# Optimization experiments

Hardware: AMD Instinct MI355X
Metric: run time of the kernel (lower is better)

Reference implementation:

```python
import jax, jax.numpy as jnp
import numpy as np

C0 = 16          # embed channels (c0) == mamba d_model
OUT_DIM = 32
D_INNER = 32     # expand * c0
D_STATE = 16
D_CONV = 4
DT_RANK = 1      # max(1, d_model // 16)
EPS = 1e-5


def setup_inputs():
    key = jax.random.key(0)
    ks = jax.random.split(key, 32)

    def n(i, shape, s):
        return (jax.random.normal(ks[i], shape) * s).astype(jnp.float32)

    inp = {
        "x": jax.random.normal(ks[0], (1, 4, 64, 64, 64), jnp.float32),
        "embed_w": n(1, (4, C0, 1, 7, 7, 7), 0.1),   # 4 per-modality conv7 stems
        "ln_g": jnp.ones((C0,), jnp.float32),
        "ln_b": jnp.zeros((C0,), jnp.float32),
        "in_proj_w": n(2, (2 * D_INNER, C0), 0.25),
        "out_proj_w": n(3, (C0, D_INNER), 0.18),
        "up_w": n(4, (C0, OUT_DIM, 2, 2, 2), 0.2),   # ConvTranspose3d k=2 s=2
    }
    for j, sfx in enumerate(["", "_b"]):             # forward / backward scan params
        b = 5 + 7 * j
        inp["conv_w" + sfx] = n(b, (D_INNER, 1, D_CONV), 0.3)
        inp["conv_b" + sfx] = n(b + 1, (D_INNER,), 0.1)
        inp["xproj_w" + sfx] = n(b + 2, (DT_RANK + 2 * D_STATE, D_INNER), 0.15)
        inp["dtproj_w" + sfx] = n(b + 3, (D_INNER, DT_RANK), 0.5)
        inp["dtproj_b" + sfx] = jnp.full((D_INNER,), -4.6, jnp.float32)  # softplus ~= 0.01
        inp["A_log" + sfx] = jnp.log(jnp.tile(jnp.arange(1, D_STATE + 1, dtype=jnp.float32), (D_INNER, 1)))
        inp["D_skip" + sfx] = jnp.ones((D_INNER,), jnp.float32)
    return inp


def _instnorm(x):
    m = jnp.mean(x, axis=(2, 3, 4), keepdims=True)
    v = jnp.mean(jnp.square(x - m), axis=(2, 3, 4), keepdims=True)
    return (x - m) / jnp.sqrt(v + EPS)


def _embed(x1, w):
    # Conv3d(1, c0, k=7, s=2, p=3, bias=False) -> InstanceNorm3d -> GELU(exact)
    y = jax.lax.conv_general_dilated(x1, w, (2, 2, 2), [(3, 3)] * 3,
                                     dimension_numbers=('NCDHW', 'OIDHW', 'NCDHW'))
    return jax.nn.gelu(_instnorm(y), approximate=False)


def _branch(u, z, cw, cb, xw, dtw, dtb, A_log, D_skip):
    # One Mamba scan branch. u, z: [B, L, Dn]
    Dn = u.shape[-1]
    uc = jax.lax.conv_general_dilated(jnp.swapaxes(u, 1, 2), cw, (1,), [(D_CONV - 1, 0)],
                                      feature_group_count=Dn,
                                      dimension_numbers=('NCH', 'OIH', 'NCH'))
    u = jax.nn.silu(jnp.swapaxes(uc + cb[None, :, None], 1, 2))       # causal dw-conv + SiLU
    xdbl = u @ xw.T                                                   # [B,L,R+2N]
    dt = jax.nn.softplus(xdbl[..., :DT_RANK] @ dtw.T + dtb)           # [B,L,Dn]
    Bm = xdbl[..., DT_RANK:DT_RANK + D_STATE]                         # [B,L,N]
    Cm = xdbl[..., DT_RANK + D_STATE:]                                # [B,L,N]
    A = -jnp.exp(A_log)                                               # [Dn,N]
    a = jnp.exp(dt[..., None] * A)                                    # [B,L,Dn,N]
    b = (dt * u)[..., None] * Bm[:, :, None, :]                       # [B,L,Dn,N]

    def comb(c1, c2):
        a1, b1 = c1
        a2, b2 = c2
        return a1 * a2, a2 * b1 + b2

    _, h = jax.lax.associative_scan(comb, (a, b), axis=1)             # h_t = a_t h_{t-1} + b_t
    y = jnp.einsum('bldn,bln->bld', h, Cm) + u * D_skip
    return y * jax.nn.silu(z)


def _bimamba(t, p):
    xz = t @ p['in_proj_w'].T
    xi, z = jnp.split(xz, 2, axis=-1)
    yf = _branch(xi, z, p['conv_w'], p['conv_b'], p['xproj_w'], p['dtproj_w'],
                 p['dtproj_b'], p['A_log'], p['D_skip'])
    yb = _branch(xi[:, ::-1], z[:, ::-1], p['conv_w_b'], p['conv_b_b'], p['xproj_w_b'],
                 p['dtproj_w_b'], p['dtproj_b_b'], p['A_log_b'], p['D_skip_b'])[:, ::-1]
    return (yf + yb) @ p['out_proj_w'].T


def _mamba_dir(x5, p):
    B, C = x5.shape[:2]
    t = jnp.swapaxes(x5.reshape(B, C, -1), 1, 2)                      # [B, L, C]
    mu = jnp.mean(t, axis=-1, keepdims=True)
    var = jnp.mean(jnp.square(t - mu), axis=-1, keepdims=True)
    t = (t - mu) / jnp.sqrt(var + EPS) * p['ln_g'] + p['ln_b']        # LayerNorm
    t = _bimamba(t, p)
    return jnp.swapaxes(t, 1, 2).reshape(x5.shape)


def _mamba_layer(x5, p):
    # tri-directional scans: (d,w,h), (w,d,h), (h,w,d) + residual
    o1 = _mamba_dir(x5, p)
    o2 = jnp.transpose(_mamba_dir(jnp.transpose(x5, (0, 1, 3, 2, 4)), p), (0, 1, 3, 2, 4))
    o3 = jnp.transpose(_mamba_dir(jnp.transpose(x5, (0, 1, 4, 3, 2)), p), (0, 1, 4, 3, 2))
    return o1 + o2 + o3 + x5


def reference(x, embed_w, ln_g, ln_b, in_proj_w, out_proj_w, up_w,
              conv_w, conv_b, xproj_w, dtproj_w, dtproj_b, A_log, D_skip,
              conv_w_b, conv_b_b, xproj_w_b, dtproj_w_b, dtproj_b_b, A_log_b, D_skip_b):
    p = dict(ln_g=ln_g, ln_b=ln_b, in_proj_w=in_proj_w, out_proj_w=out_proj_w,
             conv_w=conv_w, conv_b=conv_b, xproj_w=xproj_w, dtproj_w=dtproj_w,
             dtproj_b=dtproj_b, A_log=A_log, D_skip=D_skip,
             conv_w_b=conv_w_b, conv_b_b=conv_b_b, xproj_w_b=xproj_w_b,
             dtproj_w_b=dtproj_w_b, dtproj_b_b=dtproj_b_b, A_log_b=A_log_b,
             D_skip_b=D_skip_b)
    us = [_embed(x[:, m:m + 1], embed_w[m]) for m in range(4)]        # 4 modalities
    outs = [_mamba_layer(u, p) for u in us]
    y = outs[0] + outs[1] + outs[2] + outs[3] + us[0] + us[1] + us[2] + us[3]
    B, _, D, H, W = y.shape
    # ConvTranspose3d(c0, out_dim, k=2, s=2): each output 2x2x2 block from one input voxel
    y = jnp.einsum('bcdhw,coijk->bodihjwk', y, up_w).reshape(B, OUT_DIM, 2 * D, 2 * H, 2 * W)
    return y
```

## Files before the change

kernel.cpp:

```cpp
#include <hip/hip_runtime.h>
#include <math.h>

#define L 32768
#define CH 64
#define NC 512

#if __has_builtin(__builtin_amdgcn_exp2f)
#define EXP2(x) __builtin_amdgcn_exp2f(x)
#else
#define EXP2(x) exp2f(x)
#endif

__device__ __forceinline__ int sigma_map(int l, int perm) {
    int b2 = l >> 10, b1 = (l >> 5) & 31, b0 = l & 31;
    if (perm == 0) return (b2 << 10) | (b1 << 5) | b0;
    if (perm == 1) return (b1 << 10) | (b2 << 5) | b0;
    return (b0 << 10) | (b1 << 5) | b2;
}

__device__ __forceinline__ float silu_f(float v) {
    return v / (1.f + __expf(-v));
}
__device__ __forceinline__ float softplus_f(float x) {
    return fmaxf(x, 0.f) + log1pf(__expf(-fabsf(x)));
}

__device__ __forceinline__ float oct_sum(float x) {
    int v = __builtin_amdgcn_update_dpp(0, __float_as_int(x), 0xB1, 0xf, 0xf, true);
    x += __int_as_float(v);
    v = __builtin_amdgcn_update_dpp(0, __float_as_int(x), 0x4E, 0xf, 0xf, true);
    x += __int_as_float(v);
    v = __builtin_amdgcn_update_dpp(0, __float_as_int(x), 0x124, 0xf, 0xf, true);
    x += __int_as_float(v);
    return x;
}

__global__ __launch_bounds__(256) void k_embed(const float* __restrict__ x,
                                               const float* __restrict__ w,
                                               float* __restrict__ us) {
    __shared__ float tile[10143];
    int bx = blockIdx.x, m = blockIdx.y;
    int c = bx >> 7, sb = bx & 127;
    int zc = sb >> 2, yc0 = (sb & 3) << 3;
    const float* xin = x + m * 262144;
    int iz0 = 2 * zc - 3, iy0 = 2 * yc0 - 3;
    for (int i = threadIdx.x; i < 10143; i += 256) {
        int tz = i / 1449, r = i - tz * 1449;
        int ty = r / 69, tx = r - ty * 69;
        int gz = iz0 + tz, gy = iy0 + ty, gx = tx - 3;
        float v = 0.f;
        if ((unsigned)gz < 64u && (unsigned)gy < 64u && (unsigned)gx < 64u)
            v = xin[(gz * 64 + gy) * 64 + gx];
        tile[i] = v;
    }
    __syncthreads();
    const float* wc = w + (m * 16 + c) * 343;
    int tyl = threadIdx.x >> 5, xc = threadIdx.x & 31;
    float acc = 0.f;
    for (int kz = 0; kz < 7; ++kz)
        for (int ky = 0; ky < 7; ++ky) {
            const float* row = &tile[(kz * 21 + 2 * tyl + ky) * 69 + 2 * xc];
            const float* wr = &wc[kz * 49 + ky * 7];
            #pragma unroll
            for (int kx = 0; kx < 7; ++kx) acc += row[kx] * wr[kx];
        }
    us[(m * 16 + c) * 32768 + sb * 256 + threadIdx.x] = acc;
}

__global__ void k_instnorm_gelu(float* __restrict__ us) {
    int ch = blockIdx.x;
    float* p = us + ch * 32768;
    float s = 0.f, s2 = 0.f;
    for (int i = threadIdx.x; i < 32768; i += 256) { float v = p[i]; s += v; s2 += v * v; }
    __shared__ float rs[256], rs2[256];
    rs[threadIdx.x] = s; rs2[threadIdx.x] = s2;
    __syncthreads();
    for (int o = 128; o > 0; o >>= 1) {
        if (threadIdx.x < o) { rs[threadIdx.x] += rs[threadIdx.x + o]; rs2[threadIdx.x] += rs2[threadIdx.x + o]; }
        __syncthreads();
    }
    float mu = rs[0] * (1.f / 32768.f);
    float var = rs2[0] * (1.f / 32768.f) - mu * mu;
    float rinv = rsqrtf(var + 1e-5f);
    for (int i = threadIdx.x; i < 32768; i += 256) {
        float v = (p[i] - mu) * rinv;
        p[i] = 0.5f * v * (1.f + erff(v * 0.70710678118654752f));
    }
}

__global__ void k_transpose(const float* __restrict__ us, float* __restrict__ us_t) {
    __shared__ float tl[16][257];
    int m = blockIdx.x >> 7, t0 = (blockIdx.x & 127) << 8;
    for (int i = threadIdx.x; i < 4096; i += 256) {
        int c = i >> 8, j = i & 255;
        tl[c][j] = us[(m * 16 + c) * 32768 + t0 + j];
    }
    __syncthreads();
    for (int i = threadIdx.x; i < 4096; i += 256) {
        int j = i >> 4, c = i & 15;
        us_t[(m * 32768 + t0 + j) * 16 + c] = tl[c][j];
    }
}

__global__ __launch_bounds__(512) void k_chunkA2(
    const float* __restrict__ us_t, const float* __restrict__ ln_g, const float* __restrict__ ln_b,
    const float* __restrict__ Wip, const float* __restrict__ Wout,
    const float* __restrict__ cwA, const float* __restrict__ cbA, const float* __restrict__ xwA,
    const float* __restrict__ dtwA, const float* __restrict__ dtbA, const float* __restrict__ AlA,
    const float* __restrict__ DsA,
    const float* __restrict__ cwB, const float* __restrict__ cbB, const float* __restrict__ xwB,
    const float* __restrict__ dtwB, const float* __restrict__ dtbB, const float* __restrict__ AlB,
    const float* __restrict__ DsB,
    float* __restrict__ hst, float* __restrict__ sumdtSt,
    float* __restrict__ xd0st, _Float16* __restrict__ Csth,
    float* __restrict__ O) {
    __shared__ float sm[13376];
    float* xiT = sm;
    float* zT  = sm + 2304;
    float* syT = sm + 4480;
    float* uSh = sm + 6656;
    float* sBC = sm + 8832;
    float* xd0 = sm + 11136;
    float* G   = sm + 11200;

    int c = blockIdx.x, dir = blockIdx.y;
    int m = dir / 3, perm = dir - m * 3;
    int p0 = c * CH;
    int tid = threadIdx.x;

    for (int i = tid; i < 1024; i += 512) G[i] = Wip[i];
    if (tid < 16) G[1024 + tid] = ln_g[tid];
    else if (tid < 32) G[1024 + tid] = ln_b[tid - 16];
    __syncthreads();

    if (tid < 70) {
        int p = p0 - 3 + tid;
        if ((unsigned)p < (unsigned)L) {
            int sp = sigma_map(p, perm);
            const float4* rw = (const float4*)(us_t + (m * 32768 + sp) * 16);
            float t[16];
            ((float4*)t)[0] = rw[0]; ((float4*)t)[1] = rw[1];
            ((float4*)t)[2] = rw[2]; ((float4*)t)[3] = rw[3];
            float mu = 0.f;
            #pragma unroll
            for (int ci = 0; ci < 16; ++ci) mu += t[ci];
            mu *= (1.f / 16.f);
            float var = 0.f;
            #pragma unroll
            for (int ci = 0; ci < 16; ++ci) { float d = t[ci] - mu; var += d * d; }
            var *= (1.f / 16.f);
            float rinv = rsqrtf(var + 1e-5f);
            #pragma unroll
            for (int ci = 0; ci < 16; ++ci)
                uSh[ci * 72 + tid] = (t[ci] - mu) * rinv * G[1024 + ci] + G[1040 + ci];
        } else {
            #pragma unroll
            for (int ci = 0; ci < 16; ++ci) uSh[ci * 72 + tid] = 0.f;
        }
    }
    __syncthreads();

    for (int it = tid; it < 1152; it += 512) {
        int dd = it / 18, q = it - dd * 18;
        float ax = 0.f, ay = 0.f, az = 0.f, aw = 0.f;
        #pragma unroll
        for (int ci = 0; ci < 16; ++ci) {
            float4 tq = *(const float4*)&uSh[ci * 72 + 4 * q];
            float wv = G[dd * 16 + ci];
            ax += tq.x * wv; ay += tq.y * wv; az += tq.z * wv; aw += tq.w * wv;
        }
        int d = dd & 31;
        if (dd < 32) {
            float4 o4 = {ax, ay, az, aw};
            *(float4*)&xiT[d * 72 + 4 * q] = o4;
        } else if (q < 17) {
            float4 o4 = {silu_f(ax), silu_f(ay), silu_f(az), silu_f(aw)};
            *(float4*)&zT[d * 68 + 4 * q] = o4;
        }
    }
    __syncthreads();

    for (int b = 0; b < 2; ++b) {
        const float* cw  = b ? cwB  : cwA;
        const float* cb  = b ? cbB  : cbA;
        const float* xw  = b ? xwB  : xwA;
        const float* dtw = b ? dtwB : dtwA;
        const float* dtb = b ? dtbB : dtbA;
        const float* Al  = b ? AlB  : AlA;
        const float* Ds  = b ? DsB  : DsA;
        int chunk = b ? (NC - 1 - c) : c;
        size_t dirbIdx = (size_t)(dir * 2 + b) * NC + chunk;

        for (int i = tid; i < 1056; i += 512) G[i] = xw[i];
        if (tid < 128) G[1056 + tid] = cw[tid];
        else if (tid < 160) G[1056 + tid] = cb[tid - 128];
        __syncthreads();

        {
            int d = tid >> 4, q = tid & 15, s0 = 4 * q;
            float xr[7];
            if (b == 0) {
                #pragma unroll
                for (int j = 0; j < 7; ++j) xr[j] = xiT[d * 72 + s0 + j];
            } else {
                #pragma unroll
                for (int j = 0; j < 7; ++j) xr[j] = xiT[d * 72 + 63 - s0 + j];
            }
            float w0 = G[1056 + d * 4], w1 = G[1057 + d * 4], w2 = G[1058 + d * 4], w3 = G[1059 + d * 4];
            float bias = G[1184 + d];
            #pragma unroll
            for (int i = 0; i < 4; ++i) {
                float a;
                if (b == 0) a = bias + xr[i] * w0 + xr[i + 1] * w1 + xr[i + 2] * w2 + xr[i + 3] * w3;
                else        a = bias + xr[6 - i] * w0 + xr[5 - i] * w1 + xr[4 - i] * w2 + xr[3 - i] * w3;
                uSh[d * 68 + s0 + i] = silu_f(a);
            }
        }
        __syncthreads();

        for (int it = tid; it < 528; it += 512) {
            int j = it >> 4, q = it & 15, s0 = 4 * q;
            float ax = 0.f, ay = 0.f, az = 0.f, aw = 0.f;
            #pragma unroll
            for (int ci = 0; ci < 32; ++ci) {
                float4 uq = *(const float4*)&uSh[ci * 68 + s0];
                float wv = G[j * 32 + ci];
                ax += uq.x * wv; ay += uq.y * wv; az += uq.z * wv; aw += uq.w * wv;
            }
            if (j == 0) {
                float4 o4 = {ax, ay, az, aw};
                *(float4*)&xd0[s0] = o4;
                *(float4*)&xd0st[dirbIdx * 64 + s0] = o4;
            } else {
                int col;
                if (j < 17) { int bj = j - 1;  col = 4 * (bj >> 1) + (bj & 1); }
                else        { int cj = j - 17; col = 4 * (cj >> 1) + 2 + (cj & 1); }
                sBC[(s0 + 0) * 36 + col] = ax;
                sBC[(s0 + 1) * 36 + col] = ay;
                sBC[(s0 + 2) * 36 + col] = az;
                sBC[(s0 + 3) * 36 + col] = aw;
                if (j >= 17) {
                    int cj = j - 17;
                    Csth[(dirbIdx * 64 + s0 + 0) * 16 + cj] = (_Float16)ax;
                    Csth[(dirbIdx * 64 + s0 + 1) * 16 + cj] = (_Float16)ay;
                    Csth[(dirbIdx * 64 + s0 + 2) * 16 + cj] = (_Float16)az;
                    Csth[(dirbIdx * 64 + s0 + 3) * 16 + cj] = (_Float16)aw;
                }
            }
        }
        __syncthreads();

        for (int i = tid; i < 2048; i += 512) {
            int d2 = i >> 6, s = i & 63;
            G[d2 * 68 + s] = softplus_f(xd0[s] * dtw[d2] + dtb[d2]);
        }
        __syncthreads();

        if (tid < 256) {
            int d = tid >> 3, lane8 = tid & 7, nb = lane8 * 2;
            float kk0 = -1.44269504f * __expf(Al[d * 16 + nb + 0]);
            float kk1 = -1.44269504f * __expf(Al[d * 16 + nb + 1]);
            float Dsv = Ds[d];
            float h0 = 0.f, h1 = 0.f, cum = 0.f;
            const float* dtp = &G[d * 68];
            const float* up  = &uSh[d * 68];
            for (int s0 = 0; s0 < CH; s0 += 4) {
                float4 dt4 = *(const float4*)&dtp[s0];
                float4 u4  = *(const float4*)&up[s0];
                float pr0, pr1, pr2, pr3;
                #define CSTEP(DT, UU, SS, PR) { \
                    float w_ = (DT) * (UU); \
                    float4 bc = *(const float4*)&sBC[(SS) * 36 + 4 * lane8]; \
                    h0 = fmaf(EXP2((DT) * kk0), h0, w_ * bc.x); \
                    h1 = fmaf(EXP2((DT) * kk1), h1, w_ * bc.y); \
                    float p_ = fmaf(h1, bc.w, h0 * bc.z); \
                    cum += (DT); \
                    PR = oct_sum(p_); }
                CSTEP(dt4.x, u4.x, s0 + 0, pr0)
                CSTEP(dt4.y, u4.y, s0 + 1, pr1)
                CSTEP(dt4.z, u4.z, s0 + 2, pr2)
                CSTEP(dt4.w, u4.w, s0 + 3, pr3)
                #undef CSTEP
                if (lane8 == 0) {
                    if (b == 0) {
                        float4 o;
                        o.x = pr0 + u4.x * Dsv;
                        o.y = pr1 + u4.y * Dsv;
                        o.z = pr2 + u4.z * Dsv;
                        o.w = pr3 + u4.w * Dsv;
                        *(float4*)&syT[d * 68 + s0] = o;
                    } else {
                        float4* dst = (float4*)&syT[d * 68 + (60 - s0)];
                        float4 o = *dst;
                        o.x += pr3 + u4.w * Dsv;
                        o.y += pr2 + u4.z * Dsv;
                        o.z += pr1 + u4.y * Dsv;
                        o.w += pr0 + u4.x * Dsv;
                        *dst = o;
                    }
                }
            }
            float2 hv; hv.x = h0; hv.y = h1;
            *(float2*)&hst[dirbIdx * 512 + (size_t)(d * 16 + nb)] = hv;
            if (lane8 == 0) sumdtSt[dirbIdx * 32 + d] = cum;
        }
        __syncthreads();
    }

    for (int it = tid; it < 2048; it += 512) {
        int d = it >> 6, pl = it & 63;
        syT[d * 68 + pl] *= zT[d * 68 + pl + 3];
    }
    __syncthreads();

    if (tid < 512) G[tid] = Wout[tid];
    __syncthreads();
    for (int it = tid; it < 1024; it += 512) {
        int p = it >> 4, cc = it & 15;
        float acc = 0.f;
        #pragma unroll
        for (int d = 0; d < 32; ++d) acc += syT[d * 68 + p] * G[cc * 32 + d];
        O[((size_t)(dir * 32768 + p0 + p)) * 16 + cc] = acc;
    }
}

__global__ __launch_bounds__(512) void k_scanB(float* __restrict__ hst,
                                               const float* __restrict__ sumdtSt,
                                               const float* __restrict__ AlA,
                                               const float* __restrict__ AlB) {
    int db = blockIdx.x;
    const float* Al = (db & 1) ? AlB : AlA;
    int t = threadIdx.x, d = t >> 4;
    float A = -__expf(Al[t]);
    float* base = hst + (size_t)db * NC * 512 + t;
    const float* sb = sumdtSt + (size_t)db * NC * 32 + d;
    float H = 0.f;
    for (int c0 = 0; c0 < NC; c0 += 4) {
        float h0 = base[(c0 + 0) * 512], h1 = base[(c0 + 1) * 512];
        float h2 = base[(c0 + 2) * 512], h3 = base[(c0 + 3) * 512];
        float P0 = __expf(sb[(c0 + 0) * 32] * A);
        float P1 = __expf(sb[(c0 + 1) * 32] * A);
        float P2 = __expf(sb[(c0 + 2) * 32] * A);
        float P3 = __expf(sb[(c0 + 3) * 32] * A);
        base[(c0 + 0) * 512] = H; H = fmaf(P0, H, h0);
        base[(c0 + 1) * 512] = H; H = fmaf(P1, H, h1);
        base[(c0 + 2) * 512] = H; H = fmaf(P2, H, h2);
        base[(c0 + 3) * 512] = H; H = fmaf(P3, H, h3);
    }
}

__global__ __launch_bounds__(512) void k_fix(
    const float* __restrict__ us_t, const float* __restrict__ ln_g, const float* __restrict__ ln_b,
    const float* __restrict__ Wip, const float* __restrict__ Wout,
    const float* __restrict__ dtwA, const float* __restrict__ dtbA, const float* __restrict__ AlA,
    const float* __restrict__ dtwB, const float* __restrict__ dtbB, const float* __restrict__ AlB,
    const float* __restrict__ hst, const float* __restrict__ xd0st,
    const _Float16* __restrict__ Csth, float* __restrict__ O) {
    __shared__ float hinF[512], hinB[512];
    __shared__ float CF[1280], CB[1280];
    __shared__ float tnT[1088];
    __shared__ float sWz[512], sWout[512], sgb[32];
    __shared__ float xdF[64], xdB[64];
    __shared__ float cumB[2048];
    __shared__ float lsum[512];
    __shared__ float syC[2176];

    int c = blockIdx.x, dir = blockIdx.y;
    int m = dir / 3, perm = dir - m * 3;
    int tid = threadIdx.x;

    size_t fI = (size_t)(dir * 2 + 0) * NC + c;
    size_t bI = (size_t)(dir * 2 + 1) * NC + (NC - 1 - c);

    hinF[tid] = hst[fI * 512 + tid];
    hinB[tid] = hst[bI * 512 + tid];
    sWz[tid]  = Wip[512 + tid];
    sWout[tid] = Wout[tid];
    if (tid < 16) sgb[tid] = ln_g[tid];
    else if (tid < 32) sgb[tid] = ln_b[tid - 16];
    if (tid < 64) { xdF[tid] = xd0st[fI * 64 + tid]; xdB[tid] = xd0st[bI * 64 + tid]; }
    {
        const _Float16* cf = Csth + fI * 1024;
        const _Float16* cbp = Csth + bI * 1024;
        int i = tid, s = i >> 4, n = i & 15;
        CF[s * 20 + n] = (float)cf[i]; CB[s * 20 + n] = (float)cbp[i];
        i = tid + 512; s = i >> 4; n = i & 15;
        CF[s * 20 + n] = (float)cf[i]; CB[s * 20 + n] = (float)cbp[i];
    }
    __syncthreads();

    if (tid < 64) {
        int p = c * CH + tid;
        int sp = sigma_map(p, perm);
        const float4* rw = (const float4*)(us_t + (m * 32768 + sp) * 16);
        float t[16];
        ((float4*)t)[0] = rw[0]; ((float4*)t)[1] = rw[1];
        ((float4*)t)[2] = rw[2]; ((float4*)t)[3] = rw[3];
        float mu = 0.f;
        #pragma unroll
        for (int ci = 0; ci < 16; ++ci) mu += t[ci];
        mu *= (1.f / 16.f);
        float var = 0.f;
        #pragma unroll
        for (int ci = 0; ci < 16; ++ci) { float dd = t[ci] - mu; var += dd * dd; }
        var *= (1.f / 16.f);
        float rinv = rsqrtf(var + 1e-5f);
        #pragma unroll
        for (int ci = 0; ci < 16; ++ci)
            tnT[ci * 68 + tid] = (t[ci] - mu) * rinv * sgb[ci] + sgb[16 + ci];
    }
    __syncthreads();

    int d = tid >> 4, sq = tid & 15, s0 = 4 * sq;

    float dwF = dtwA[d], dbF = dtbA[d];
    float dF0 = softplus_f(xdF[s0 + 0] * dwF + dbF);
    float dF1 = softplus_f(xdF[s0 + 1] * dwF + dbF);
    float dF2 = softplus_f(xdF[s0 + 2] * dwF + dbF);
    float dF3 = softplus_f(xdF[s0 + 3] * dwF + dbF);
    lsum[tid] = ((dF0 + dF1) + (dF2 + dF3));
    __syncthreads();
    float baseF = 0.f;
    #pragma unroll
    for (int k = 0; k < 16; ++k) { float v = lsum[d * 16 + k]; baseF += (k < sq) ? v : 0.f; }
    float cF0 = baseF + dF0, cF1 = cF0 + dF1, cF2 = cF1 + dF2, cF3 = cF2 + dF3;
    __syncthreads();

    float dwB = dtwB[d], dbB = dtbB[d];
    float dB0 = softplus_f(xdB[s0 + 0] * dwB + dbB);
    float dB1 = softplus_f(xdB[s0 + 1] * dwB + dbB);
    float dB2 = softplus_f(xdB[s0 + 2] * dwB + dbB);
    float dB3 = softplus_f(xdB[s0 + 3] * dwB + dbB);
    lsum[tid] = ((dB0 + dB1) + (dB2 + dB3));
    __syncthreads();
    float baseB = 0.f;
    #pragma unroll
    for (int k = 0; k < 16; ++k) { float v = lsum[d * 16 + k]; baseB += (k < sq) ? v : 0.f; }
    {
        float c0v = baseB + dB0, c1v = c0v + dB1, c2v = c1v + dB2, c3v = c2v + dB3;
        float4 o4 = {c0v, c1v, c2v, c3v};
        *(float4*)&cumB[d * 64 + s0] = o4;
    }
    __syncthreads();

    {
        float z0 = 0.f, z1 = 0.f, z2 = 0.f, z3 = 0.f;
        #pragma unroll
        for (int ci = 0; ci < 16; ++ci) {
            float4 tq = *(const float4*)&tnT[ci * 68 + s0];
            float wv = sWz[d * 16 + ci];
            z0 += tq.x * wv; z1 += tq.y * wv; z2 += tq.z * wv; z3 += tq.w * wv;
        }
        z0 = silu_f(z0); z1 = silu_f(z1); z2 = silu_f(z2); z3 = silu_f(z3);
        float zv[4] = {z0, z1, z2, z3};
        float cFv[4] = {cF0, cF1, cF2, cF3};

        float e0F = __expf(AlA[d * 16]);
        float e0B = __expf(AlB[d * 16]);
        const float* hFp = &hinF[d * 16];
        const float* hBp = &hinB[d * 16];

        float out4[4];
        #pragma unroll
        for (int i = 0; i < 4; ++i) {
            int p = s0 + i;
            int sb = 63 - p;
            float rF = __expf(-cFv[i] * e0F);
            float rB = __expf(-cumB[d * 64 + sb] * e0B);
            const float* Crf = &CF[p * 20];
            const float* Crb = &CB[sb * 20];
            float accF = 0.f, accB = 0.f;
            #pragma unroll
            for (int n = 15; n >= 0; --n) {
                accF = fmaf(rF, accF, hFp[n] * Crf[n]);
                accB = fmaf(rB, accB, hBp[n] * Crb[n]);
            }
            out4[i] = (rF * accF + rB * accB) * zv[i];
        }
        float4 o4 = {out4[0], out4[1], out4[2], out4[3]};
        *(float4*)&syC[d * 68 + s0] = o4;
    }
    __syncthreads();

    for (int it = tid; it < 1024; it += 512) {
        int p = it >> 4, cc2 = it & 15;
        float acc = 0.f;
        #pragma unroll
        for (int dd = 0; dd < 32; ++dd) acc += syC[dd * 68 + p] * sWout[cc2 * 32 + dd];
        size_t oi = ((size_t)(dir * 32768 + c * CH + p)) * 16 + cc2;
        O[oi] += acc;
    }
}

__global__ void k_accum(const float* __restrict__ us_t, const float* __restrict__ O,
                        float* __restrict__ acc_t) {
    int it = blockIdx.x * 256 + threadIdx.x;
    int sp = it >> 2, q = (it & 3) << 2;
    float ax = 0.f, ay = 0.f, az = 0.f, aw = 0.f;
    #pragma unroll
    for (int mm = 0; mm < 4; ++mm) {
        float4 v = *(const float4*)&us_t[(mm * 32768 + sp) * 16 + q];
        ax += 2.f * v.x; ay += 2.f * v.y; az += 2.f * v.z; aw += 2.f * v.w;
    }
    #pragma unroll
    for (int perm = 0; perm < 3; ++perm) {
        int l = sigma_map(sp, perm);
        #pragma unroll
        for (int mm = 0; mm < 4; ++mm) {
            int dir = mm * 3 + perm;
            float4 v = *(const float4*)&O[((size_t)(dir * 32768 + l)) * 16 + q];
            ax += v.x; ay += v.y; az += v.z; aw += v.w;
        }
    }
    float4 o4 = {ax, ay, az, aw};
    *(float4*)&acc_t[sp * 16 + q] = o4;
}

__global__ void k_up(const float* __restrict__ acc_t, const float* __restrict__ upw,
                     float* __restrict__ out) {
    __shared__ float w[4096];
    for (int i = threadIdx.x; i < 4096; i += 256) w[i] = upw[i];
    __syncthreads();
    int e = blockIdx.x * 256 + threadIdx.x;
    int o = e >> 17;
    int r2 = e & 131071;
    int Dz = r2 >> 11, Hy = (r2 >> 5) & 63, Wp = r2 & 31;
    int sp = ((Dz >> 1) << 10) | ((Hy >> 1) << 5) | Wp;
    int wbase = (((Dz & 1) << 2) | ((Hy & 1) << 1));
    const float* arow = &acc_t[sp * 16];
    float v0 = 0.f, v1 = 0.f;
    #pragma unroll
    for (int c = 0; c < 16; ++c) {
        float a = arow[c];
        const float* wr = &w[(c * 32 + o) * 8 + wbase];
        v0 += a * wr[0];
        v1 += a * wr[1];
    }
    float2 ov; ov.x = v0; ov.y = v1;
    *(float2*)&out[((o * 64 + Dz) * 64 + Hy) * 64 + 2 * Wp] = ov;
}

extern "C" void kernel_launch(void* const* d_in, const int* in_sizes, int n_in,
                              void* d_out, int out_size, void* d_ws, size_t ws_size,
                              hipStream_t stream) {
    (void)in_sizes; (void)n_in; (void)out_size; (void)ws_size;
    const float* x    = (const float*)d_in[0];
    const float* embw = (const float*)d_in[1];
    const float* ln_g = (const float*)d_in[2];
    const float* ln_b = (const float*)d_in[3];
    const float* Wip  = (const float*)d_in[4];
    const float* Wout = (const float*)d_in[5];
    const float* upw  = (const float*)d_in[6];
    const float* cwA  = (const float*)d_in[7];
    const float* cbA  = (const float*)d_in[8];
    const float* xwA  = (const float*)d_in[9];
    const float* dtwA = (const float*)d_in[10];
    const float* dtbA = (const float*)d_in[11];
    const float* AlA  = (const float*)d_in[12];
    const float* DsA  = (const float*)d_in[13];
    const float* cwB  = (const float*)d_in[14];
    const float* cbB  = (const float*)d_in[15];
    const float* xwB  = (const float*)d_in[16];
    const float* dtwB = (const float*)d_in[17];
    const float* dtbB = (const float*)d_in[18];
    const float* AlB  = (const float*)d_in[19];
    const float* DsB  = (const float*)d_in[20];

    float* ws = (float*)d_ws;
    float*    us      = ws;
    float*    xd0st   = ws;
    float*    sumdtSt = ws + 786432;
    float*    acc_t   = ws + 1179648;
    float*    us_t    = ws + 2097152;
    float*    hst     = ws + 4194304;
    float*    O       = ws + 10485760;
    _Float16* Csth    = (_Float16*)(ws + 16777216);

    k_embed<<<dim3(2048, 4), 256, 0, stream>>>(x, embw, us);
    k_instnorm_gelu<<<64, 256, 0, stream>>>(us);
    k_transpose<<<512, 256, 0, stream>>>(us, us_t);
    k_chunkA2<<<dim3(NC, 12), 512, 0, stream>>>(us_t, ln_g, ln_b, Wip, Wout,
                                                cwA, cbA, xwA, dtwA, dtbA, AlA, DsA,
                                                cwB, cbB, xwB, dtwB, dtbB, AlB, DsB,
                                                hst, sumdtSt, xd0st, Csth, O);
    k_scanB<<<24, 512, 0, stream>>>(hst, sumdtSt, AlA, AlB);
    k_fix<<<dim3(NC, 12), 512, 0, stream>>>(us_t, ln_g, ln_b, Wip, Wout,
                                            dtwA, dtbA, AlA, dtwB, dtbB, AlB,
                                            hst, xd0st, Csth, O);
    k_accum<<<512, 256, 0, stream>>>(us_t, O, acc_t);
    k_up<<<16384, 256, 0, stream>>>(acc_t, upw, (float*)d_out);
}
```

Measured before the change: 772.4 us.

## Precompute LayerNorm and in_proj once in fp16, store chunk states in fp16

A new k_proj kernel replaces the transpose and computes LayerNorm plus the x/z input projection once per voxel, storing xi and silu(z) as fp16. The chunk and fix kernels then load these instead of recomputing the norm and projection for each of the 12 directions. Inter-chunk hidden states are also stored in fp16, the conv stem tile is padded for float2 loads, and accum/up now read channel-major data. This trades redundant compute and bandwidth for reduced-precision intermediates, which may affect accuracy.

```diff
diff --git a/kernel.cpp b/kernel.cpp
--- a/kernel.cpp
+++ b/kernel.cpp
@@ -38,15 +38,15 @@
 __global__ __launch_bounds__(256) void k_embed(const float* __restrict__ x,
                                                const float* __restrict__ w,
                                                float* __restrict__ us) {
-    __shared__ float tile[10143];
+    __shared__ float tile[10290];
     int bx = blockIdx.x, m = blockIdx.y;
     int c = bx >> 7, sb = bx & 127;
     int zc = sb >> 2, yc0 = (sb & 3) << 3;
     const float* xin = x + m * 262144;
     int iz0 = 2 * zc - 3, iy0 = 2 * yc0 - 3;
-    for (int i = threadIdx.x; i < 10143; i += 256) {
-        int tz = i / 1449, r = i - tz * 1449;
-        int ty = r / 69, tx = r - ty * 69;
+    for (int i = threadIdx.x; i < 10290; i += 256) {
+        int tz = i / 1470, r = i - tz * 1470;
+        int ty = r / 70, tx = r - ty * 70;
         int gz = iz0 + tz, gy = iy0 + ty, gx = tx - 3;
         float v = 0.f;
         if ((unsigned)gz < 64u && (unsigned)gy < 64u && (unsigned)gx < 64u)
@@ -59,10 +59,19 @@
     float acc = 0.f;
     for (int kz = 0; kz < 7; ++kz)
         for (int ky = 0; ky < 7; ++ky) {
-            const float* row = &tile[(kz * 21 + 2 * tyl + ky) * 69 + 2 * xc];
+            const float* row = &tile[(kz * 21 + 2 * tyl + ky) * 70 + 2 * xc];
             const float* wr = &wc[kz * 49 + ky * 7];
-            #pragma unroll
-            for (int kx = 0; kx < 7; ++kx) acc += row[kx] * wr[kx];
+            float2 r01 = *(const float2*)(row);
+            float2 r23 = *(const float2*)(row + 2);
+            float2 r45 = *(const float2*)(row + 4);
+            float r6 = row[6];
+            acc += r01.x * wr[0];
+            acc += r01.y * wr[1];
+            acc += r23.x * wr[2];
+            acc += r23.y * wr[3];
+            acc += r45.x * wr[4];
+            acc += r45.y * wr[5];
+            acc += r6 * wr[6];
         }
     us[(m * 16 + c) * 32768 + sb * 256 + threadIdx.x] = acc;
 }
@@ -88,30 +97,77 @@
     }
 }
 
-__global__ void k_transpose(const float* __restrict__ us, float* __restrict__ us_t) {
+__global__ __launch_bounds__(256) void k_proj(const float* __restrict__ us,
+                                              const float* __restrict__ ln_g, const float* __restrict__ ln_b,
+                                              const float* __restrict__ Wip,
+                                              _Float16* __restrict__ xi_g, _Float16* __restrict__ zg) {
     __shared__ float tl[16][257];
+    __shared__ float W[1024];
+    __shared__ float gb[32];
     int m = blockIdx.x >> 7, t0 = (blockIdx.x & 127) << 8;
+    for (int i = threadIdx.x; i < 1024; i += 256) W[i] = Wip[i];
+    if (threadIdx.x < 16) gb[threadIdx.x] = ln_g[threadIdx.x];
+    else if (threadIdx.x < 32) gb[threadIdx.x] = ln_b[threadIdx.x - 16];
     for (int i = threadIdx.x; i < 4096; i += 256) {
         int c = i >> 8, j = i & 255;
-        tl[c][j] = us[(m * 16 + c) * 32768 + t0 + j];
-    }
-    __syncthreads();
-    for (int i = threadIdx.x; i < 4096; i += 256) {
-        int j = i >> 4, c = i & 15;
-        us_t[(m * 32768 + t0 + j) * 16 + c] = tl[c][j];
-    }
+        tl[c][j] = us[(size_t)(m * 16 + c) * 32768 + t0 + j];
+    }
+    __syncthreads();
+    int tid = threadIdx.x;
+    float t[16];
+    float mu = 0.f;
+    #pragma unroll
+    for (int c = 0; c < 16; ++c) { t[c] = tl[c][tid]; mu += t[c]; }
+    mu *= (1.f / 16.f);
+    float var = 0.f;
+    #pragma unroll
+    for (int c = 0; c < 16; ++c) { float d = t[c] - mu; var += d * d; }
+    var *= (1.f / 16.f);
+    float rinv = rsqrtf(var + 1e-5f);
+    #pragma unroll
+    for (int c = 0; c < 16; ++c) t[c] = (t[c] - mu) * rinv * gb[c] + gb[16 + c];
+
+    alignas(16) _Float16 ox[32];
+    alignas(16) _Float16 oz[32];
+    #pragma unroll
+    for (int dd = 0; dd < 32; ++dd) {
+        const float4* wq = (const float4*)&W[dd * 16];
+        float4 w0 = wq[0], w1 = wq[1], w2 = wq[2], w3 = wq[3];
+        float a = t[0] * w0.x + t[1] * w0.y + t[2] * w0.z + t[3] * w0.w
+                + t[4] * w1.x + t[5] * w1.y + t[6] * w1.z + t[7] * w1.w
+                + t[8] * w2.x + t[9] * w2.y + t[10] * w2.z + t[11] * w2.w
+                + t[12] * w3.x + t[13] * w3.y + t[14] * w3.z + t[15] * w3.w;
+        ox[dd] = (_Float16)a;
+    }
+    #pragma unroll
+    for (int dd = 0; dd < 32; ++dd) {
+        const float4* wq = (const float4*)&W[(32 + dd) * 16];
+        float4 w0 = wq[0], w1 = wq[1], w2 = wq[2], w3 = wq[3];
+        float a = t[0] * w0.x + t[1] * w0.y + t[2] * w0.z + t[3] * w0.w
+                + t[4] * w1.x + t[5] * w1.y + t[6] * w1.z + t[7] * w1.w
+                + t[8] * w2.x + t[9] * w2.y + t[10] * w2.z + t[11] * w2.w
+                + t[12] * w3.x + t[13] * w3.y + t[14] * w3.z + t[15] * w3.w;
+        oz[dd] = (_Float16)silu_f(a);
+    }
+    size_t row = (size_t)m * 32768 + t0 + tid;
+    uint4* xd = (uint4*)(xi_g + row * 32);
+    uint4* zd = (uint4*)(zg + row * 32);
+    const uint4* pox = (const uint4*)ox;
+    const uint4* poz = (const uint4*)oz;
+    xd[0] = pox[0]; xd[1] = pox[1]; xd[2] = pox[2]; xd[3] = pox[3];
+    zd[0] = poz[0]; zd[1] = poz[1]; zd[2] = poz[2]; zd[3] = poz[3];
 }
 
 __global__ __launch_bounds__(512) void k_chunkA2(
-    const float* __restrict__ us_t, const float* __restrict__ ln_g, const float* __restrict__ ln_b,
-    const float* __restrict__ Wip, const float* __restrict__ Wout,
+    const _Float16* __restrict__ xi_g, const _Float16* __restrict__ zg,
+    const float* __restrict__ Wout,
     const float* __restrict__ cwA, const float* __restrict__ cbA, const float* __restrict__ xwA,
     const float* __restrict__ dtwA, const float* __restrict__ dtbA, const float* __restrict__ AlA,
     const float* __restrict__ DsA,
     const float* __restrict__ cwB, const float* __restrict__ cbB, const float* __restrict__ xwB,
     const float* __restrict__ dtwB, const float* __restrict__ dtbB, const float* __restrict__ AlB,
     const float* __restrict__ DsB,
-    float* __restrict__ hst, float* __restrict__ sumdtSt,
+    _Float16* __restrict__ hstH, float* __restrict__ sumdtSt,
     float* __restrict__ xd0st, _Float16* __restrict__ Csth,
     float* __restrict__ O) {
     __shared__ float sm[13376];
@@ -128,55 +184,29 @@
     int p0 = c * CH;
     int tid = threadIdx.x;
 
-    for (int i = tid; i < 1024; i += 512) G[i] = Wip[i];
-    if (tid < 16) G[1024 + tid] = ln_g[tid];
-    else if (tid < 32) G[1024 + tid] = ln_b[tid - 16];
-    __syncthreads();
-
-    if (tid < 70) {
-        int p = p0 - 3 + tid;
+    for (int it = tid; it < 560; it += 512) {
+        int row = it >> 3, dq = (it & 7) << 2;
+        int p = p0 - 3 + row;
+        float v0 = 0.f, v1 = 0.f, v2 = 0.f, v3 = 0.f;
         if ((unsigned)p < (unsigned)L) {
             int sp = sigma_map(p, perm);
-            const float4* rw = (const float4*)(us_t + (m * 32768 + sp) * 16);
-            float t[16];
-            ((float4*)t)[0] = rw[0]; ((float4*)t)[1] = rw[1];
-            ((float4*)t)[2] = rw[2]; ((float4*)t)[3] = rw[3];
-            float mu = 0.f;
-            #pragma unroll
-            for (int ci = 0; ci < 16; ++ci) mu += t[ci];
-            mu *= (1.f / 16.f);
-            float var = 0.f;
-            #pragma unroll
-            for (int ci = 0; ci < 16; ++ci) { float d = t[ci] - mu; var += d * d; }
-            var *= (1.f / 16.f);
-            float rinv = rsqrtf(var + 1e-5f);
-            #pragma unroll
-            for (int ci = 0; ci < 16; ++ci)
-                uSh[ci * 72 + tid] = (t[ci] - mu) * rinv * G[1024 + ci] + G[1040 + ci];
-        } else {
-            #pragma unroll
-            for (int ci = 0; ci < 16; ++ci) uSh[ci * 72 + tid] = 0.f;
-        }
-    }
-    __syncthreads();
-
-    for (int it = tid; it < 1152; it += 512) {
-        int dd = it / 18, q = it - dd * 18;
-        float ax = 0.f, ay = 0.f, az = 0.f, aw = 0.f;
-        #pragma unroll
-        for (int ci = 0; ci < 16; ++ci) {
-            float4 tq = *(const float4*)&uSh[ci * 72 + 4 * q];
-            float wv = G[dd * 16 + ci];
-            ax += tq.x * wv; ay += tq.y * wv; az += tq.z * wv; aw += tq.w * wv;
-        }
-        int d = dd & 31;
-        if (dd < 32) {
-            float4 o4 = {ax, ay, az, aw};
-            *(float4*)&xiT[d * 72 + 4 * q] = o4;
-        } else if (q < 17) {
-            float4 o4 = {silu_f(ax), silu_f(ay), silu_f(az), silu_f(aw)};
-            *(float4*)&zT[d * 68 + 4 * q] = o4;
-        }
+            const _Float16* xr = xi_g + ((size_t)m * 32768 + sp) * 32 + dq;
+            v0 = (float)xr[0]; v1 = (float)xr[1]; v2 = (float)xr[2]; v3 = (float)xr[3];
+        }
+        xiT[(dq + 0) * 72 + row] = v0;
+        xiT[(dq + 1) * 72 + row] = v1;
+        xiT[(dq + 2) * 72 + row] = v2;
+        xiT[(dq + 3) * 72 + row] = v3;
+    }
+    {
+        int row = tid >> 3, dq = (tid & 7) << 2;
+        int p = p0 + row;
+        int sp = sigma_map(p, perm);
+        const _Float16* zr = zg + ((size_t)m * 32768 + sp) * 32 + dq;
+        zT[(dq + 0) * 68 + row + 3] = (float)zr[0];
+        zT[(dq + 1) * 68 + row + 3] = (float)zr[1];
+        zT[(dq + 2) * 68 + row + 3] = (float)zr[2];
+        zT[(dq + 3) * 68 + row + 3] = (float)zr[3];
     }
     __syncthreads();
 
@@ -300,8 +330,9 @@
                     }
                 }
             }
-            float2 hv; hv.x = h0; hv.y = h1;
-            *(float2*)&hst[dirbIdx * 512 + (size_t)(d * 16 + nb)] = hv;
+            _Float16* hh = hstH + dirbIdx * 512 + (size_t)(d * 16 + nb);
+            hh[0] = (_Float16)h0;
+            hh[1] = (_Float16)h1;
             if (lane8 == 0) sumdtSt[dirbIdx * 32 + d] = cum;
         }
         __syncthreads();
@@ -324,7 +355,7 @@
     }
 }
 
-__global__ __launch_bounds__(512) void k_scanB(float* __restrict__ hst,
+__global__ __launch_bounds__(512) void k_scanB(_Float16* __restrict__ hstH,
                                                const float* __restrict__ sumdtSt,
                                                const float* __restrict__ AlA,
                                                const float* __restrict__ AlB) {
@@ -332,34 +363,33 @@
     const float* Al = (db & 1) ? AlB : AlA;
     int t = threadIdx.x, d = t >> 4;
     float A = -__expf(Al[t]);
-    float* base = hst + (size_t)db * NC * 512 + t;
+    _Float16* base = hstH + (size_t)db * NC * 512 + t;
     const float* sb = sumdtSt + (size_t)db * NC * 32 + d;
     float H = 0.f;
     for (int c0 = 0; c0 < NC; c0 += 4) {
-        float h0 = base[(c0 + 0) * 512], h1 = base[(c0 + 1) * 512];
-        float h2 = base[(c0 + 2) * 512], h3 = base[(c0 + 3) * 512];
+        float h0 = (float)base[(c0 + 0) * 512], h1 = (float)base[(c0 + 1) * 512];
+        float h2 = (float)base[(c0 + 2) * 512], h3 = (float)base[(c0 + 3) * 512];
         float P0 = __expf(sb[(c0 + 0) * 32] * A);
         float P1 = __expf(sb[(c0 + 1) * 32] * A);
         float P2 = __expf(sb[(c0 + 2) * 32] * A);
         float P3 = __expf(sb[(c0 + 3) * 32] * A);
-        base[(c0 + 0) * 512] = H; H = fmaf(P0, H, h0);
-        base[(c0 + 1) * 512] = H; H = fmaf(P1, H, h1);
-        base[(c0 + 2) * 512] = H; H = fmaf(P2, H, h2);
-        base[(c0 + 3) * 512] = H; H = fmaf(P3, H, h3);
+        base[(c0 + 0) * 512] = (_Float16)H; H = fmaf(P0, H, h0);
+        base[(c0 + 1) * 512] = (_Float16)H; H = fmaf(P1, H, h1);
+        base[(c0 + 2) * 512] = (_Float16)H; H = fmaf(P2, H, h2);
+        base[(c0 + 3) * 512] = (_Float16)H; H = fmaf(P3, H, h3);
     }
 }
 
 __global__ __launch_bounds__(512) void k_fix(
-    const float* __restrict__ us_t, const float* __restrict__ ln_g, const float* __restrict__ ln_b,
-    const float* __restrict__ Wip, const float* __restrict__ Wout,
+    const _Float16* __restrict__ zg, const float* __restrict__ Wout,
     const float* __restrict__ dtwA, const float* __restrict__ dtbA, const float* __restrict__ AlA,
     const float* __restrict__ dtwB, const float* __restrict__ dtbB, const float* __restrict__ AlB,
-    const float* __restrict__ hst, const float* __restrict__ xd0st,
+    const _Float16* __restrict__ hstH, const float* __restrict__ xd0st,
     const _Float16* __restrict__ Csth, float* __restrict__ O) {
     __shared__ float hinF[512], hinB[512];
     __shared__ float CF[1280], CB[1280];
-    __shared__ float tnT[1088];
-    __shared__ float sWz[512], sWout[512], sgb[32];
+    __shared__ float zL[2112];
+    __shared__ float sWout[512];
     __shared__ float xdF[64], xdB[64];
     __shared__ float cumB[2048];
     __shared__ float lsum[512];
@@ -372,12 +402,9 @@
     size_t fI = (size_t)(dir * 2 + 0) * NC + c;
     size_t bI = (size_t)(dir * 2 + 1) * NC + (NC - 1 - c);
 
-    hinF[tid] = hst[fI * 512 + tid];
-    hinB[tid] = hst[bI * 512 + tid];
-    sWz[tid]  = Wip[512 + tid];
+    hinF[tid] = (float)hstH[fI * 512 + tid];
+    hinB[tid] = (float)hstH[bI * 512 + tid];
     sWout[tid] = Wout[tid];
-    if (tid < 16) sgb[tid] = ln_g[tid];
-    else if (tid < 32) sgb[tid] = ln_b[tid - 16];
     if (tid < 64) { xdF[tid] = xd0st[fI * 64 + tid]; xdB[tid] = xd0st[bI * 64 + tid]; }
     {
         const _Float16* cf = Csth + fI * 1024;
@@ -387,27 +414,15 @@
         i = tid + 512; s = i >> 4; n = i & 15;
         CF[s * 20 + n] = (float)cf[i]; CB[s * 20 + n] = (float)cbp[i];
     }
-    __syncthreads();
-
-    if (tid < 64) {
-        int p = c * CH + tid;
+    {
+        int row = tid >> 3, dq = (tid & 7) << 2;
+        int p = c * CH + row;
         int sp = sigma_map(p, perm);
-        const float4* rw = (const float4*)(us_t + (m * 32768 + sp) * 16);
-        float t[16];
-        ((float4*)t)[0] = rw[0]; ((float4*)t)[1] = rw[1];
-        ((float4*)t)[2] = rw[2]; ((float4*)t)[3] = rw[3];
-        float mu = 0.f;
-        #pragma unroll
-        for (int ci = 0; ci < 16; ++ci) mu += t[ci];
-        mu *= (1.f / 16.f);
-        float var = 0.f;
-        #pragma unroll
-        for (int ci = 0; ci < 16; ++ci) { float dd = t[ci] - mu; var += dd * dd; }
-        var *= (1.f / 16.f);
-        float rinv = rsqrtf(var + 1e-5f);
-        #pragma unroll
-        for (int ci = 0; ci < 16; ++ci)
-            tnT[ci * 68 + tid] = (t[ci] - mu) * rinv * sgb[ci] + sgb[16 + ci];
+        const _Float16* zr = zg + ((size_t)m * 32768 + sp) * 32 + dq;
+        zL[row * 33 + dq + 0] = (float)zr[0];
+        zL[row * 33 + dq + 1] = (float)zr[1];
+        zL[row * 33 + dq + 2] = (float)zr[2];
+        zL[row * 33 + dq + 3] = (float)zr[3];
     }
     __syncthreads();
 
@@ -444,21 +459,11 @@
     __syncthreads();
 
     {
-        float z0 = 0.f, z1 = 0.f, z2 = 0.f, z3 = 0.f;
-        #pragma unroll
-        for (int ci = 0; ci < 16; ++ci) {
-            float4 tq = *(const float4*)&tnT[ci * 68 + s0];
-            float wv = sWz[d * 16 + ci];
-            z0 += tq.x * wv; z1 += tq.y * wv; z2 += tq.z * wv; z3 += tq.w * wv;
-        }
-        z0 = silu_f(z0); z1 = silu_f(z1); z2 = silu_f(z2); z3 = silu_f(z3);
-        float zv[4] = {z0, z1, z2, z3};
-        float cFv[4] = {cF0, cF1, cF2, cF3};
-
         float e0F = __expf(AlA[d * 16]);
         float e0B = __expf(AlB[d * 16]);
         const float* hFp = &hinF[d * 16];
         const float* hBp = &hinB[d * 16];
+        float cFv[4] = {cF0, cF1, cF2, cF3};
 
         float out4[4];
         #pragma unroll
@@ -475,7 +480,8 @@
                 accF = fmaf(rF, accF, hFp[n] * Crf[n]);
                 accB = fmaf(rB, accB, hBp[n] * Crb[n]);
             }
-            out4[i] = (rF * accF + rB * accB) * zv[i];
+            float zv = zL[p * 33 + d];
+            out4[i] = (rF * accF + rB * accB) * zv;
         }
         float4 o4 = {out4[0], out4[1], out4[2], out4[3]};
         *(float4*)&syC[d * 68 + s0] = o4;
@@ -492,15 +498,18 @@
     }
 }
 
-__global__ void k_accum(const float* __restrict__ us_t, const float* __restrict__ O,
-                        float* __restrict__ acc_t) {
+__global__ void k_accum(const float* __restrict__ us, const float* __restrict__ O,
+                        float* __restrict__ acc) {
     int it = blockIdx.x * 256 + threadIdx.x;
     int sp = it >> 2, q = (it & 3) << 2;
-    float ax = 0.f, ay = 0.f, az = 0.f, aw = 0.f;
+    float a0 = 0.f, a1 = 0.f, a2 = 0.f, a3 = 0.f;
     #pragma unroll
     for (int mm = 0; mm < 4; ++mm) {
-        float4 v = *(const float4*)&us_t[(mm * 32768 + sp) * 16 + q];
-        ax += 2.f * v.x; ay += 2.f * v.y; az += 2.f * v.z; aw += 2.f * v.w;
+        const float* up = us + (size_t)(mm * 16 + q) * 32768 + sp;
+        a0 += 2.f * up[0];
+        a1 += 2.f * up[32768];
+        a2 += 2.f * up[65536];
+        a3 += 2.f * up[98304];
     }
     #pragma unroll
     for (int perm = 0; perm < 3; ++perm) {
@@ -509,14 +518,16 @@
         for (int mm = 0; mm < 4; ++mm) {
             int dir = mm * 3 + perm;
             float4 v = *(const float4*)&O[((size_t)(dir * 32768 + l)) * 16 + q];
-            ax += v.x; ay += v.y; az += v.z; aw += v.w;
-        }
-    }
-    float4 o4 = {ax, ay, az, aw};
-    *(float4*)&acc_t[sp * 16 + q] = o4;
-}
-
-__global__ void k_up(const float* __restrict__ acc_t, const float* __restrict__ upw,
+            a0 += v.x; a1 += v.y; a2 += v.z; a3 += v.w;
+        }
+    }
+    acc[(size_t)(q + 0) * 32768 + sp] = a0;
+    acc[(size_t)(q + 1) * 32768 + sp] = a1;
+    acc[(size_t)(q + 2) * 32768 + sp] = a2;
+    acc[(size_t)(q + 3) * 32768 + sp] = a3;
+}
+
+__global__ void k_up(const float* __restrict__ acc, const float* __restrict__ upw,
                      float* __restrict__ out) {
     __shared__ float w[4096];
     for (int i = threadIdx.x; i < 4096; i += 256) w[i] = upw[i];
@@ -527,11 +538,10 @@
     int Dz = r2 >> 11, Hy = (r2 >> 5) & 63, Wp = r2 & 31;
     int sp = ((Dz >> 1) << 10) | ((Hy >> 1) << 5) | Wp;
     int wbase = (((Dz & 1) << 2) | ((Hy & 1) << 1));
-    const float* arow = &acc_t[sp * 16];
     float v0 = 0.f, v1 = 0.f;
     #pragma unroll
     for (int c = 0; c < 16; ++c) {
-        float a = arow[c];
+        float a = acc[(size_t)c * 32768 + sp];
         const float* wr = &w[(c * 32 + o) * 8 + wbase];
         v0 += a * wr[0];
         v1 += a * wr[1];
@@ -568,25 +578,26 @@
 
     float* ws = (float*)d_ws;
     float*    us      = ws;
-    float*    xd0st   = ws;
-    float*    sumdtSt = ws + 786432;
-    float*    acc_t   = ws + 1179648;
-    float*    us_t    = ws + 2097152;
-    float*    hst     = ws + 4194304;
-    float*    O       = ws + 10485760;
-    _Float16* Csth    = (_Float16*)(ws + 16777216);
+    _Float16* xi_g    = (_Float16*)(ws + 2097152);
+    _Float16* zg      = (_Float16*)(ws + 4194304);
+    _Float16* hstH    = (_Float16*)(ws + 6291456);
+    float*    sumdtSt = ws + 9437184;
+    float*    xd0st   = ws + 9830400;
+    float*    accb    = ws + 9830400;
+    _Float16* Csth    = (_Float16*)(ws + 10616832);
+    float*    O       = ws + 16908288;
 
     k_embed<<<dim3(2048, 4), 256, 0, stream>>>(x, embw, us);
     k_instnorm_gelu<<<64, 256, 0, stream>>>(us);
-    k_transpose<<<512, 256, 0, stream>>>(us, us_t);
-    k_chunkA2<<<dim3(NC, 12), 512, 0, stream>>>(us_t, ln_g, ln_b, Wip, Wout,
+    k_proj<<<512, 256, 0, stream>>>(us, ln_g, ln_b, Wip, xi_g, zg);
+    k_chunkA2<<<dim3(NC, 12), 512, 0, stream>>>(xi_g, zg, Wout,
                                                 cwA, cbA, xwA, dtwA, dtbA, AlA, DsA,
                                                 cwB, cbB, xwB, dtwB, dtbB, AlB, DsB,
-                                                hst, sumdtSt, xd0st, Csth, O);
-    k_scanB<<<24, 512, 0, stream>>>(hst, sumdtSt, AlA, AlB);
-    k_fix<<<dim3(NC, 12), 512, 0, stream>>>(us_t, ln_g, ln_b, Wip, Wout,
+                                                hstH, sumdtSt, xd0st, Csth, O);
+    k_scanB<<<24, 512, 0, stream>>>(hstH, sumdtSt, AlA, AlB);
+    k_fix<<<dim3(NC, 12), 512, 0, stream>>>(zg, Wout,
                                             dtwA, dtbA, AlA, dtwB, dtbB, AlB,
-                                            hst, xd0st, Csth, O);
-    k_accum<<<512, 256, 0, stream>>>(us_t, O, acc_t);
-    k_up<<<16384, 256, 0, stream>>>(acc_t, upw, (float*)d_out);
-}
+                                            hstH, xd0st, Csth, O);
+    k_accum<<<512, 256, 0, stream>>>(us, O, accb);
+    k_up<<<16384, 256, 0, stream>>>(accb, upw, (float*)d_out);
+}
```

New measurement: 756.7 us, median of 2. -2.0%, faster.
